# Kernel optimization log

Measured on AMD Instinct MI355X. Metric: run time of the kernel, lower is better.

The kernel has to match this reference:

```python
import jax, jax.numpy as jnp
import numpy as np

B, E, H, NY, NX = 16, 128, 4, 32, 32


def setup_inputs() -> dict:
    key = jax.random.key(0)
    ks = jax.random.split(key, 7)
    w = lambda k, shape: jax.random.normal(k, shape, jnp.float32) * 0.02
    return {
        "x": jax.random.normal(ks[0], (B, E, NY, NX), jnp.float32),
        "Wk": w(ks[1], (E, E)), "bk": jnp.zeros((E,), jnp.float32),
        "Wq": w(ks[2], (E, E)), "bq": jnp.zeros((E,), jnp.float32),
        "Wv": w(ks[3], (E, E)), "bv": jnp.zeros((E,), jnp.float32),
        "Wu": w(ks[4], (E, E)), "bu": jnp.zeros((E,), jnp.float32),
        "pos_enc": w(ks[5], (H, (2 * NY - 1) * (2 * NX - 1))),
    }


def _conv1x1(x, W, b):
    # 1x1 conv == channel-mixing linear: (B,C,y,x) -> (B,O,y,x)
    return jnp.einsum('bcyx,oc->boyx', x, W) + b[None, :, None, None]


def _rel_indices(ny, nx):
    y = jnp.arange(ny)
    x = jnp.arange(nx)
    y1, x1, y2, x2 = jnp.meshgrid(y, x, y, x, indexing='ij')
    idx = (y1 - y2 + ny - 1) * (2 * nx - 1) + (x1 - x2 + nx - 1)
    return idx.reshape(ny * nx, ny * nx)  # (N, N)


def reference(x, Wk, bk, Wq, bq, Wv, bv, Wu, bu, pos_enc):
    b, e, ny, nx = x.shape
    h = pos_enc.shape[0]
    hc = e // h
    n = ny * nx
    scale = hc ** (-0.5)

    keys = _conv1x1(x, Wk, bk).reshape(b, h, hc, n)
    queries = _conv1x1(x, Wq, bq).reshape(b, h, hc, n)
    values = _conv1x1(x, Wv, bv).reshape(b, h, hc, n)

    # att[b,h,k,q] = sum_c keys[b,h,c,k] * queries[b,h,c,q]
    att = jnp.einsum('bhck,bhcq->bhkq', keys, queries) * scale

    # gathered relative position bias: (H, N, N)
    idx = _rel_indices(ny, nx)
    rel = pos_enc[:, idx]
    att = att + rel[None]

    # softmax over the key axis (dim=-2), as in the original
    att = jax.nn.softmax(att, axis=-2)

    out = jnp.einsum('bhck,bhkq->bhcq', values, att).reshape(b, e, ny, nx)
    return _conv1x1(out, Wu, bu)
```

## Files before the change

kernel.cpp:

```cpp
#include <hip/hip_runtime.h>
#include <hip/hip_bf16.h>

#define BN 16
#define EN 128
#define HN 4
#define HCN 32
#define NN 1024
#define POSN 3969

typedef short short8 __attribute__((ext_vector_type(8)));
typedef float f32x4 __attribute__((ext_vector_type(4)));

#define MFMA16(a, b, c) __builtin_amdgcn_mfma_f32_16x16x32_bf16((a), (b), (c), 0, 0, 0)

union Frag {
  short8 s8;
  uint2 u2[2];
  unsigned int u[4];
  unsigned short us[8];
};

__device__ __forceinline__ unsigned short bfbits(float x) {
  union { __hip_bfloat16 h; unsigned short u; } c;
  c.h = __float2bfloat16(x);
  return c.u;
}

__device__ __forceinline__ unsigned int pk2(float lo, float hi) {
  union { __hip_bfloat162 h2; unsigned int u; } c;
  c.h2 = __float22bfloat162_rn(make_float2(lo, hi));
  return c.u;
}

__global__ __launch_bounds__(256) void conv_qkv_mfma(
    const float* __restrict__ x,
    const float* __restrict__ Wk, const float* __restrict__ bk, __hip_bfloat16* __restrict__ kb,
    const float* __restrict__ Wq, const float* __restrict__ bq, __hip_bfloat16* __restrict__ qb,
    const float* __restrict__ Wv, const float* __restrict__ bv, __hip_bfloat16* __restrict__ vb)
{
  const int z = blockIdx.z;
  const float* W; const float* bias; __hip_bfloat16* out;
  if (z == 0)      { W = Wk; bias = bk; out = kb; }
  else if (z == 1) { W = Wq; bias = bq; out = qb; }
  else             { W = Wv; bias = bv; out = vb; }

  const int n0 = blockIdx.x * 64;
  const int bb = blockIdx.y;
  const int t = threadIdx.x, w = t >> 6, l = t & 63;
  const int l15 = l & 15, lq = l >> 4;

  __shared__ unsigned short xs[64][132];

  {
    const float* xb = x + (size_t)bb * EN * NN + n0;
    const int n = t & 63, cg = (t >> 6) * 4;
#pragma unroll
    for (int i = 0; i < 8; ++i) {
      const int cb = cg + i * 16;
      float a0 = xb[(size_t)(cb + 0) * NN + n];
      float a1 = xb[(size_t)(cb + 1) * NN + n];
      float a2 = xb[(size_t)(cb + 2) * NN + n];
      float a3 = xb[(size_t)(cb + 3) * NN + n];
      uint2 v; v.x = pk2(a0, a1); v.y = pk2(a2, a3);
      *(uint2*)&xs[n][cb] = v;
    }
  }

  Frag wf[2][4];
#pragma unroll
  for (int r = 0; r < 2; ++r) {
    const int o = (w * 2 + r) * 16 + l15;
#pragma unroll
    for (int ks = 0; ks < 4; ++ks) {
      const float* wp = W + (size_t)o * EN + ks * 32 + lq * 4;
      float4 wa = *(const float4*)wp;
      float4 wb2 = *(const float4*)(wp + 16);
      Frag f;
      f.u[0] = pk2(wa.x, wa.y);  f.u[1] = pk2(wa.z, wa.w);
      f.u[2] = pk2(wb2.x, wb2.y); f.u[3] = pk2(wb2.z, wb2.w);
      wf[r][ks] = f;
    }
  }
  __syncthreads();

  f32x4 acc[2][4];
#pragma unroll
  for (int r = 0; r < 2; ++r)
#pragma unroll
    for (int nt = 0; nt < 4; ++nt) acc[r][nt] = 0.f;

#pragma unroll
  for (int ks = 0; ks < 4; ++ks) {
#pragma unroll
    for (int nt = 0; nt < 4; ++nt) {
      Frag xf;
      xf.u2[0] = *(const uint2*)&xs[nt * 16 + l15][ks * 32 + lq * 4];
      xf.u2[1] = *(const uint2*)&xs[nt * 16 + l15][ks * 32 + lq * 4 + 16];
      if (z < 2) {
        acc[0][nt] = MFMA16(wf[0][ks].s8, xf.s8, acc[0][nt]);
        acc[1][nt] = MFMA16(wf[1][ks].s8, xf.s8, acc[1][nt]);
      } else {
        acc[0][nt] = MFMA16(xf.s8, wf[0][ks].s8, acc[0][nt]);
        acc[1][nt] = MFMA16(xf.s8, wf[1][ks].s8, acc[1][nt]);
      }
    }
  }

  if (z < 2) {
#pragma unroll
    for (int r = 0; r < 2; ++r) {
      const int ob = (w * 2 + r) * 16 + lq * 4;
      const int hh = ob >> 5;
      const int pofs = hh * 32 + ((ob >> 2) & 3) * 8 + ((ob & 16) ? 4 : 0);
      float4 b4 = *(const float4*)(bias + ob);
#pragma unroll
      for (int nt = 0; nt < 4; ++nt) {
        const int n = n0 + nt * 16 + l15;
        f32x4 a = acc[r][nt];
        uint2 o2;
        o2.x = pk2(a[0] + b4.x, a[1] + b4.y);
        o2.y = pk2(a[2] + b4.z, a[3] + b4.w);
        *(uint2*)(out + (size_t)(bb * NN + n) * 128 + pofs) = o2;
      }
    }
  } else {
#pragma unroll
    for (int r = 0; r < 2; ++r) {
      const int o = (w * 2 + r) * 16 + l15;
      const int c = o & 31, hh = o >> 5;
      const float bsc = bias[o];
#pragma unroll
      for (int nt = 0; nt < 4; ++nt) {
        const int nb = n0 + nt * 16 + lq * 4;
        const int kbk = nb >> 5, k32 = nb & 31;
        const int pofs = ((k32 >> 2) & 3) * 8 + ((k32 & 16) ? 4 : 0);
        f32x4 a = acc[r][nt];
        uint2 o2;
        o2.x = pk2(a[0] + bsc, a[1] + bsc);
        o2.y = pk2(a[2] + bsc, a[3] + bsc);
        *(uint2*)(out + ((size_t)((bb * 4 + hh) * 32 + c) * 32 + kbk) * 32 + pofs) = o2;
      }
    }
  }
}

__global__ __launch_bounds__(256) void bias_kernel(
    const float* __restrict__ pos, unsigned short* __restrict__ bias)
{
  const int gid = blockIdx.x * 256 + threadIdx.x;
  const int l = gid & 63;
  const int t2 = gid >> 6;
  const int dxi = t2 % 3;
  const int dy31 = (t2 / 3) % 63;
  const int h = t2 / 189;
  const int rowk0 = (l >> 4) * 4, colq = l & 15;
  const float log2e = 1.4426950408889634f;

  unsigned int bits[4];
#pragma unroll
  for (int j = 0; j < 4; ++j) {
    const int dx = (dxi - 1) * 16 + rowk0 + j - colq + 31;
    bits[j] = (unsigned int)bfbits(pos[h * POSN + dy31 * 63 + dx] * log2e);
  }
  uint2 o;
  o.x = bits[0] | (bits[1] << 16);
  o.y = bits[2] | (bits[3] << 16);
  *(uint2*)(bias + (size_t)gid * 4) = o;
}

__global__ __launch_bounds__(256, 4) void attn_mfma_kernel(
    const __hip_bfloat16* __restrict__ kp,
    const __hip_bfloat16* __restrict__ qp,
    const __hip_bfloat16* __restrict__ vp,
    const unsigned short* __restrict__ bias,
    float* __restrict__ Op,
    float* __restrict__ lp)
{
  const int bx = blockIdx.x;
  const int qi = bx & 7, s = bx >> 3;
  const int h = blockIdx.y, b = blockIdx.z;
  const int t = threadIdx.x, w = t >> 6, l = t & 63;
  const int l15 = l & 15, lq = l >> 4;

  __shared__ Frag Kf[2][4][64];
  __shared__ Frag Vf[2][4][64];

  const __hip_bfloat16* kStage = kp + (size_t)b * 131072 + h * 32 + lq * 8
                                 + (size_t)(w * 16 + l15) * 128;
  const __hip_bfloat16* vStage = vp + (size_t)(b * 4 + h) * 32768
                                 + (size_t)((w >> 1) * 16 + l15) * 1024
                                 + (w & 1) * 32 + lq * 8;
  const unsigned short* biasB = bias + (size_t)h * 48384 + l * 4;

  const int qt0 = qi * 8 + w * 2;
  Frag qf[2];
  qf[0] = *(const Frag*)(qp + (size_t)(b * 1024 + (qt0 + 0) * 16 + l15) * 128 + h * 32 + lq * 8);
  qf[1] = *(const Frag*)(qp + (size_t)(b * 1024 + (qt0 + 1) * 16 + l15) * 128 + h * 32 + lq * 8);
  const int qy[2] = {(qt0 + 0) >> 1, (qt0 + 1) >> 1};
  const int qx1[2] = {(qt0 + 0) & 1, (qt0 + 1) & 1};

  {
    const int chg = s * 8;
    Kf[0][w][l] = *(const Frag*)(kStage + (size_t)chg * 64 * 128);
    Vf[0][w][l] = *(const Frag*)(vStage + chg * 64);
  }
  __syncthreads();

  f32x4 O[2][2];
#pragma unroll
  for (int mt = 0; mt < 2; ++mt)
#pragma unroll
    for (int nt = 0; nt < 2; ++nt) O[mt][nt] = 0.f;
  float lacc[2] = {0.f, 0.f};

  const float SCALE2 = 0.17677669529663687f * 1.4426950408889634f;

  for (int c8 = 0; c8 < 8; ++c8) {
    const int buf = c8 & 1;
    const int chg = s * 8 + c8;

    Frag kn, vn;
    if (c8 < 7) {
      kn = *(const Frag*)(kStage + (size_t)(chg + 1) * 64 * 128);
      vn = *(const Frag*)(vStage + (chg + 1) * 64);
    }

    uint2 bw[2][4];
#pragma unroll
    for (int nt = 0; nt < 2; ++nt)
#pragma unroll
      for (int kt = 0; kt < 4; ++kt) {
        const int ktg = chg * 4 + kt;
        const int off = ((ktg >> 1) - qy[nt] + 31) * 768 + ((ktg & 1) - qx1[nt] + 1) * 256;
        bw[nt][kt] = *(const uint2*)(biasB + off);
      }

    short8 ka[4], va[4];
#pragma unroll
    for (int kt = 0; kt < 4; ++kt) ka[kt] = Kf[buf][kt][l].s8;
#pragma unroll
    for (int i = 0; i < 4; ++i) va[i] = Vf[buf][i][l].s8;

#pragma unroll
    for (int nt = 0; nt < 2; ++nt) {
      f32x4 S[4];
#pragma unroll
      for (int kt = 0; kt < 4; ++kt) {
        f32x4 z = 0.f;
        S[kt] = MFMA16(ka[kt], qf[nt].s8, z);
      }
      float p[16];
#pragma unroll
      for (int kt = 0; kt < 4; ++kt) {
        const float b0 = __uint_as_float(bw[nt][kt].x << 16);
        const float b1 = __uint_as_float(bw[nt][kt].x & 0xffff0000u);
        const float b2 = __uint_as_float(bw[nt][kt].y << 16);
        const float b3 = __uint_as_float(bw[nt][kt].y & 0xffff0000u);
        p[kt * 4 + 0] = exp2f(fmaf(S[kt][0], SCALE2, b0));
        p[kt * 4 + 1] = exp2f(fmaf(S[kt][1], SCALE2, b1));
        p[kt * 4 + 2] = exp2f(fmaf(S[kt][2], SCALE2, b2));
        p[kt * 4 + 3] = exp2f(fmaf(S[kt][3], SCALE2, b3));
      }
#pragma unroll
      for (int e = 0; e < 16; ++e) lacc[nt] += p[e];

      Frag B0, B1;
      B0.u[0] = pk2(p[0], p[1]);   B0.u[1] = pk2(p[2], p[3]);
      B0.u[2] = pk2(p[4], p[5]);   B0.u[3] = pk2(p[6], p[7]);
      B1.u[0] = pk2(p[8], p[9]);   B1.u[1] = pk2(p[10], p[11]);
      B1.u[2] = pk2(p[12], p[13]); B1.u[3] = pk2(p[14], p[15]);

      O[0][nt] = MFMA16(va[0], B0.s8, O[0][nt]);
      O[0][nt] = MFMA16(va[1], B1.s8, O[0][nt]);
      O[1][nt] = MFMA16(va[2], B0.s8, O[1][nt]);
      O[1][nt] = MFMA16(va[3], B1.s8, O[1][nt]);
    }

    if (c8 < 7) {
      Kf[buf ^ 1][w][l] = kn;
      Vf[buf ^ 1][w][l] = vn;
      __syncthreads();
    }
  }

#pragma unroll
  for (int nt = 0; nt < 2; ++nt) {
    lacc[nt] += __shfl_xor(lacc[nt], 16);
    lacc[nt] += __shfl_xor(lacc[nt], 32);
  }
  if (lq == 0) {
#pragma unroll
    for (int nt = 0; nt < 2; ++nt)
      lp[((size_t)(s * 16 + b) * 4 + h) * 1024 + (qt0 + nt) * 16 + l15] = lacc[nt];
  }

  float* ob = Op + (size_t)s * 2097152 + ((size_t)b * EN + h * HCN) * NN;
#pragma unroll
  for (int mt = 0; mt < 2; ++mt)
#pragma unroll
    for (int nt = 0; nt < 2; ++nt)
#pragma unroll
      for (int j = 0; j < 4; ++j)
        ob[(size_t)(mt * 16 + lq * 4 + j) * NN + (qt0 + nt) * 16 + l15] = O[mt][nt][j];
}

__global__ __launch_bounds__(256) void conv_final_mfma(
    const float* __restrict__ Op,
    const float* __restrict__ lp,
    const float* __restrict__ Wu, const float* __restrict__ bu,
    float* __restrict__ out)
{
  const int n0 = blockIdx.x * 32;
  const int bb = blockIdx.y;
  const int t = threadIdx.x, w = t >> 6, l = t & 63;
  const int l15 = l & 15, lq = l >> 4;

  __shared__ unsigned short ahi[32][132];
  __shared__ unsigned short alo[32][132];

  {
    const float* O0 = Op + (size_t)bb * (EN * NN) + n0;
    const float* O1 = O0 + 2097152;
    const float* l0 = lp + (size_t)bb * 4096 + n0;
    const float* l1 = l0 + 65536;
    const int n = t & 31, cg = (t >> 5) * 4;
#pragma unroll
    for (int i = 0; i < 4; ++i) {
      const int cb = cg + i * 32;
      const float rl = 1.0f / (l0[i * 1024 + n] + l1[i * 1024 + n]);
      float a[4]; unsigned short hb[4]; float lf[4];
#pragma unroll
      for (int j = 0; j < 4; ++j) {
        a[j] = (O0[(size_t)(cb + j) * NN + n] + O1[(size_t)(cb + j) * NN + n]) * rl;
        __hip_bfloat16 hh = __float2bfloat16(a[j]);
        union { __hip_bfloat16 h; unsigned short u; } c; c.h = hh;
        hb[j] = c.u;
        lf[j] = a[j] - __bfloat162float(hh);
      }
      uint2 uh; uh.x = hb[0] | ((unsigned int)hb[1] << 16);
                uh.y = hb[2] | ((unsigned int)hb[3] << 16);
      uint2 ul; ul.x = pk2(lf[0], lf[1]); ul.y = pk2(lf[2], lf[3]);
      *(uint2*)&ahi[n][cb] = uh;
      *(uint2*)&alo[n][cb] = ul;
    }
  }

  Frag whi[2][4], wlo[2][4];
#pragma unroll
  for (int r = 0; r < 2; ++r) {
    const int o = (w * 2 + r) * 16 + l15;
#pragma unroll
    for (int ks = 0; ks < 4; ++ks) {
      const float* wp = Wu + (size_t)o * EN + ks * 32 + lq * 4;
      float4 wa = *(const float4*)wp;
      float4 wb2 = *(const float4*)(wp + 16);
      float v[8] = {wa.x, wa.y, wa.z, wa.w, wb2.x, wb2.y, wb2.z, wb2.w};
      unsigned short hb[8]; float lf[8];
#pragma unroll
      for (int e = 0; e < 8; ++e) {
        __hip_bfloat16 hh = __float2bfloat16(v[e]);
        union { __hip_bfloat16 h; unsigned short u; } c; c.h = hh;
        hb[e] = c.u;
        lf[e] = v[e] - __bfloat162float(hh);
      }
      Frag fh, fl;
#pragma unroll
      for (int e = 0; e < 4; ++e)
        fh.u[e] = hb[2 * e] | ((unsigned int)hb[2 * e + 1] << 16);
      fl.u[0] = pk2(lf[0], lf[1]); fl.u[1] = pk2(lf[2], lf[3]);
      fl.u[2] = pk2(lf[4], lf[5]); fl.u[3] = pk2(lf[6], lf[7]);
      whi[r][ks] = fh; wlo[r][ks] = fl;
    }
  }
  __syncthreads();

  f32x4 acc[2][2];
#pragma unroll
  for (int r = 0; r < 2; ++r)
#pragma unroll
    for (int nt = 0; nt < 2; ++nt) acc[r][nt] = 0.f;

#pragma unroll
  for (int ks = 0; ks < 4; ++ks) {
#pragma unroll
    for (int nt = 0; nt < 2; ++nt) {
      Frag ah, al;
      ah.u2[0] = *(const uint2*)&ahi[nt * 16 + l15][ks * 32 + lq * 4];
      ah.u2[1] = *(const uint2*)&ahi[nt * 16 + l15][ks * 32 + lq * 4 + 16];
      al.u2[0] = *(const uint2*)&alo[nt * 16 + l15][ks * 32 + lq * 4];
      al.u2[1] = *(const uint2*)&alo[nt * 16 + l15][ks * 32 + lq * 4 + 16];
#pragma unroll
      for (int r = 0; r < 2; ++r) {
        acc[r][nt] = MFMA16(ah.s8, whi[r][ks].s8, acc[r][nt]);
        acc[r][nt] = MFMA16(al.s8, whi[r][ks].s8, acc[r][nt]);
        acc[r][nt] = MFMA16(ah.s8, wlo[r][ks].s8, acc[r][nt]);
      }
    }
  }

#pragma unroll
  for (int r = 0; r < 2; ++r) {
    const int o = (w * 2 + r) * 16 + l15;
    const float bo = bu[o];
#pragma unroll
    for (int nt = 0; nt < 2; ++nt) {
      const int nb = n0 + nt * 16 + lq * 4;
      f32x4 a = acc[r][nt];
      float4 res = make_float4(a[0] + bo, a[1] + bo, a[2] + bo, a[3] + bo);
      *(float4*)(out + ((size_t)bb * EN + o) * NN + nb) = res;
    }
  }
}

extern "C" void kernel_launch(void* const* d_in, const int* in_sizes, int n_in,
                              void* d_out, int out_size, void* d_ws, size_t ws_size,
                              hipStream_t stream)
{
  const float* x   = (const float*)d_in[0];
  const float* Wk  = (const float*)d_in[1];
  const float* bk  = (const float*)d_in[2];
  const float* Wq  = (const float*)d_in[3];
  const float* bq  = (const float*)d_in[4];
  const float* Wv  = (const float*)d_in[5];
  const float* bv  = (const float*)d_in[6];
  const float* Wu  = (const float*)d_in[7];
  const float* bu  = (const float*)d_in[8];
  const float* pos = (const float*)d_in[9];

  char* ws = (char*)d_ws;
  __hip_bfloat16* kb = (__hip_bfloat16*)(ws);
  __hip_bfloat16* qb = (__hip_bfloat16*)(ws + (size_t)4194304);
  __hip_bfloat16* vb = (__hip_bfloat16*)(ws + (size_t)8388608);
  unsigned short* bias = (unsigned short*)(ws + (size_t)12582912);
  float* lp = (float*)(ws + (size_t)13107200);
  float* Op = (float*)(ws + (size_t)13631488);

  bias_kernel<<<189, 256, 0, stream>>>(pos, bias);

  dim3 g1(16, BN, 3);
  conv_qkv_mfma<<<g1, 256, 0, stream>>>(x, Wk, bk, kb, Wq, bq, qb, Wv, bv, vb);

  dim3 g2(16, HN, BN);
  attn_mfma_kernel<<<g2, 256, 0, stream>>>(kb, qb, vb, bias, Op, lp);

  dim3 g3(32, BN);
  conv_final_mfma<<<g3, 256, 0, stream>>>(Op, lp, Wu, bu, (float*)d_out);
}
```

Measured before the change: 63.64 us.

## Precompute weight fragments in prep kernel and compute softmax denominator with MFMA

Measured after the change: 58.11 us. 8.7% less time.

```diff
diff --git a/kernel.cpp b/kernel.cpp
--- a/kernel.cpp
+++ b/kernel.cpp
@@ -32,17 +32,82 @@
   return c.u;
 }
 
+__global__ __launch_bounds__(256) void prep_kernel(
+    const float* __restrict__ pos,
+    const float* __restrict__ Wk, const float* __restrict__ Wq,
+    const float* __restrict__ Wv, const float* __restrict__ Wu,
+    unsigned short* __restrict__ bias, Frag* __restrict__ wtab,
+    Frag* __restrict__ whitab, Frag* __restrict__ wlotab)
+{
+  const int b0 = blockIdx.x, t = threadIdx.x;
+  if (b0 < 189) {
+    const int gid = b0 * 256 + t;
+    const int l = gid & 63;
+    const int t2 = gid >> 6;
+    const int dxi = t2 % 3;
+    const int dy31 = (t2 / 3) % 63;
+    const int h = t2 / 189;
+    const int rowk0 = (l >> 4) * 4, colq = l & 15;
+    const float log2e = 1.4426950408889634f;
+    unsigned int bits[4];
+#pragma unroll
+    for (int j = 0; j < 4; ++j) {
+      const int dx = (dxi - 1) * 16 + rowk0 + j - colq + 31;
+      bits[j] = (unsigned int)bfbits(pos[h * POSN + dy31 * 63 + dx] * log2e);
+    }
+    uint2 o;
+    o.x = bits[0] | (bits[1] << 16);
+    o.y = bits[2] | (bits[3] << 16);
+    *(uint2*)(bias + (size_t)gid * 4) = o;
+  } else if (b0 < 213) {
+    const int fid = (b0 - 189) * 256 + t;
+    const int z = fid >> 11, rem = fid & 2047;
+    const int ot = rem >> 8, ks = (rem >> 6) & 3, l = rem & 63;
+    const float* W = (z == 0) ? Wk : (z == 1) ? Wq : Wv;
+    const int o = ot * 16 + (l & 15), lq = l >> 4;
+    const float* wp = W + (size_t)o * EN + ks * 32 + lq * 4;
+    float4 wa = *(const float4*)wp;
+    float4 wb2 = *(const float4*)(wp + 16);
+    Frag f;
+    f.u[0] = pk2(wa.x, wa.y);   f.u[1] = pk2(wa.z, wa.w);
+    f.u[2] = pk2(wb2.x, wb2.y); f.u[3] = pk2(wb2.z, wb2.w);
+    wtab[fid] = f;
+  } else {
+    const int fid = (b0 - 213) * 256 + t;
+    const int ot = fid >> 8, ks = (fid >> 6) & 3, l = fid & 63;
+    const int o = ot * 16 + (l & 15), lq = l >> 4;
+    const float* wp = Wu + (size_t)o * EN + ks * 32 + lq * 4;
+    float4 wa = *(const float4*)wp;
+    float4 wb2 = *(const float4*)(wp + 16);
+    float v[8] = {wa.x, wa.y, wa.z, wa.w, wb2.x, wb2.y, wb2.z, wb2.w};
+    unsigned short hb[8]; float lf[8];
+#pragma unroll
+    for (int e = 0; e < 8; ++e) {
+      __hip_bfloat16 hh = __float2bfloat16(v[e]);
+      union { __hip_bfloat16 h; unsigned short u; } c; c.h = hh;
+      hb[e] = c.u;
+      lf[e] = v[e] - __bfloat162float(hh);
+    }
+    Frag fh, fl;
+#pragma unroll
+    for (int e = 0; e < 4; ++e)
+      fh.u[e] = hb[2 * e] | ((unsigned int)hb[2 * e + 1] << 16);
+    fl.u[0] = pk2(lf[0], lf[1]); fl.u[1] = pk2(lf[2], lf[3]);
+    fl.u[2] = pk2(lf[4], lf[5]); fl.u[3] = pk2(lf[6], lf[7]);
+    whitab[fid] = fh;
+    wlotab[fid] = fl;
+  }
+}
+
 __global__ __launch_bounds__(256) void conv_qkv_mfma(
-    const float* __restrict__ x,
-    const float* __restrict__ Wk, const float* __restrict__ bk, __hip_bfloat16* __restrict__ kb,
-    const float* __restrict__ Wq, const float* __restrict__ bq, __hip_bfloat16* __restrict__ qb,
-    const float* __restrict__ Wv, const float* __restrict__ bv, __hip_bfloat16* __restrict__ vb)
+    const float* __restrict__ x, const Frag* __restrict__ wtab,
+    const float* __restrict__ bk, __hip_bfloat16* __restrict__ kb,
+    const float* __restrict__ bq, __hip_bfloat16* __restrict__ qb,
+    const float* __restrict__ bv, __hip_bfloat16* __restrict__ vb)
 {
   const int z = blockIdx.z;
-  const float* W; const float* bias; __hip_bfloat16* out;
-  if (z == 0)      { W = Wk; bias = bk; out = kb; }
-  else if (z == 1) { W = Wq; bias = bq; out = qb; }
-  else             { W = Wv; bias = bv; out = vb; }
+  const float* bias = (z == 0) ? bk : (z == 1) ? bq : bv;
+  __hip_bfloat16* out = (z == 0) ? kb : (z == 1) ? qb : vb;
 
   const int n0 = blockIdx.x * 64;
   const int bb = blockIdx.y;
@@ -68,19 +133,10 @@
 
   Frag wf[2][4];
 #pragma unroll
-  for (int r = 0; r < 2; ++r) {
-    const int o = (w * 2 + r) * 16 + l15;
-#pragma unroll
-    for (int ks = 0; ks < 4; ++ks) {
-      const float* wp = W + (size_t)o * EN + ks * 32 + lq * 4;
-      float4 wa = *(const float4*)wp;
-      float4 wb2 = *(const float4*)(wp + 16);
-      Frag f;
-      f.u[0] = pk2(wa.x, wa.y);  f.u[1] = pk2(wa.z, wa.w);
-      f.u[2] = pk2(wb2.x, wb2.y); f.u[3] = pk2(wb2.z, wb2.w);
-      wf[r][ks] = f;
-    }
-  }
+  for (int r = 0; r < 2; ++r)
+#pragma unroll
+    for (int ks = 0; ks < 4; ++ks)
+      wf[r][ks] = wtab[(((size_t)z * 8 + (w * 2 + r)) * 4 + ks) * 64 + l];
   __syncthreads();
 
   f32x4 acc[2][4];
@@ -142,30 +198,6 @@
       }
     }
   }
-}
-
-__global__ __launch_bounds__(256) void bias_kernel(
-    const float* __restrict__ pos, unsigned short* __restrict__ bias)
-{
-  const int gid = blockIdx.x * 256 + threadIdx.x;
-  const int l = gid & 63;
-  const int t2 = gid >> 6;
-  const int dxi = t2 % 3;
-  const int dy31 = (t2 / 3) % 63;
-  const int h = t2 / 189;
-  const int rowk0 = (l >> 4) * 4, colq = l & 15;
-  const float log2e = 1.4426950408889634f;
-
-  unsigned int bits[4];
-#pragma unroll
-  for (int j = 0; j < 4; ++j) {
-    const int dx = (dxi - 1) * 16 + rowk0 + j - colq + 31;
-    bits[j] = (unsigned int)bfbits(pos[h * POSN + dy31 * 63 + dx] * log2e);
-  }
-  uint2 o;
-  o.x = bits[0] | (bits[1] << 16);
-  o.y = bits[2] | (bits[3] << 16);
-  *(uint2*)(bias + (size_t)gid * 4) = o;
 }
 
 __global__ __launch_bounds__(256, 4) void attn_mfma_kernel(
@@ -182,15 +214,15 @@
   const int t = threadIdx.x, w = t >> 6, l = t & 63;
   const int l15 = l & 15, lq = l >> 4;
 
-  __shared__ Frag Kf[2][4][64];
-  __shared__ Frag Vf[2][4][64];
-
-  const __hip_bfloat16* kStage = kp + (size_t)b * 131072 + h * 32 + lq * 8
-                                 + (size_t)(w * 16 + l15) * 128;
-  const __hip_bfloat16* vStage = vp + (size_t)(b * 4 + h) * 32768
-                                 + (size_t)((w >> 1) * 16 + l15) * 1024
-                                 + (w & 1) * 32 + lq * 8;
+  __shared__ Frag Kf[2][8][64];
+  __shared__ Frag Vf[2][8][64];
+
+  const __hip_bfloat16* kBase = kp + (size_t)b * 131072 + h * 32 + (size_t)l15 * 128 + lq * 8;
+  const __hip_bfloat16* vBase = vp + (size_t)((b * 4 + h) * 32 + l15) * 1024 + lq * 8;
   const unsigned short* biasB = bias + (size_t)h * 48384 + l * 4;
+
+#define KADDR(CHG, KT) ((const Frag*)(kBase + (size_t)((CHG) * 128 + (KT) * 16) * 128))
+#define VADDR(CHG, SL) ((const Frag*)(vBase + (size_t)((SL) >> 2) * 16384 + ((CHG) * 4 + ((SL) & 3)) * 32))
 
   const int qt0 = qi * 8 + w * 2;
   Frag qf[2];
@@ -200,9 +232,11 @@
   const int qx1[2] = {(qt0 + 0) & 1, (qt0 + 1) & 1};
 
   {
-    const int chg = s * 8;
-    Kf[0][w][l] = *(const Frag*)(kStage + (size_t)chg * 64 * 128);
-    Vf[0][w][l] = *(const Frag*)(vStage + chg * 64);
+    const int chg = s * 4;
+    Kf[0][w][l]     = *KADDR(chg, w);
+    Kf[0][w + 4][l] = *KADDR(chg, w + 4);
+    Vf[0][w][l]     = *VADDR(chg, w);
+    Vf[0][w + 4][l] = *VADDR(chg, w + 4);
   }
   __syncthreads();
 
@@ -211,87 +245,98 @@
   for (int mt = 0; mt < 2; ++mt)
 #pragma unroll
     for (int nt = 0; nt < 2; ++nt) O[mt][nt] = 0.f;
-  float lacc[2] = {0.f, 0.f};
+  f32x4 Lacc[2]; Lacc[0] = 0.f; Lacc[1] = 0.f;
+
+  Frag ones;
+  ones.u[0] = 0x3F803F80u; ones.u[1] = 0x3F803F80u;
+  ones.u[2] = 0x3F803F80u; ones.u[3] = 0x3F803F80u;
 
   const float SCALE2 = 0.17677669529663687f * 1.4426950408889634f;
 
-  for (int c8 = 0; c8 < 8; ++c8) {
-    const int buf = c8 & 1;
-    const int chg = s * 8 + c8;
-
-    Frag kn, vn;
-    if (c8 < 7) {
-      kn = *(const Frag*)(kStage + (size_t)(chg + 1) * 64 * 128);
-      vn = *(const Frag*)(vStage + (chg + 1) * 64);
-    }
-
-    uint2 bw[2][4];
+  for (int c4 = 0; c4 < 4; ++c4) {
+    const int buf = c4 & 1;
+    const int chg = s * 4 + c4;
+
+    Frag kn[2], vn[2];
+    if (c4 < 3) {
+      kn[0] = *KADDR(chg + 1, w);
+      kn[1] = *KADDR(chg + 1, w + 4);
+      vn[0] = *VADDR(chg + 1, w);
+      vn[1] = *VADDR(chg + 1, w + 4);
+    }
+
+#pragma unroll
+    for (int hh2 = 0; hh2 < 2; ++hh2) {
+      short8 ka[4], va[4];
+#pragma unroll
+      for (int kt = 0; kt < 4; ++kt) ka[kt] = Kf[buf][hh2 * 4 + kt][l].s8;
+#pragma unroll
+      for (int mt = 0; mt < 2; ++mt)
+#pragma unroll
+        for (int kh = 0; kh < 2; ++kh)
+          va[mt * 2 + kh] = Vf[buf][mt * 4 + hh2 * 2 + kh][l].s8;
+
+#pragma unroll
+      for (int nt = 0; nt < 2; ++nt) {
+        uint2 bw[4];
+#pragma unroll
+        for (int kt = 0; kt < 4; ++kt) {
+          const int ktg = chg * 8 + hh2 * 4 + kt;
+          const int off = ((ktg >> 1) - qy[nt] + 31) * 768 + ((ktg & 1) - qx1[nt] + 1) * 256;
+          bw[kt] = *(const uint2*)(biasB + off);
+        }
+
+        __builtin_amdgcn_s_setprio(1);
+        f32x4 S[4];
+#pragma unroll
+        for (int kt = 0; kt < 4; ++kt) {
+          f32x4 z = 0.f;
+          S[kt] = MFMA16(ka[kt], qf[nt].s8, z);
+        }
+        __builtin_amdgcn_s_setprio(0);
+
+        Frag B0, B1;
+#pragma unroll
+        for (int kt = 0; kt < 4; ++kt) {
+          const float b0 = __uint_as_float(bw[kt].x << 16);
+          const float b1 = __uint_as_float(bw[kt].x & 0xffff0000u);
+          const float b2 = __uint_as_float(bw[kt].y << 16);
+          const float b3 = __uint_as_float(bw[kt].y & 0xffff0000u);
+          float p0 = exp2f(fmaf(S[kt][0], SCALE2, b0));
+          float p1 = exp2f(fmaf(S[kt][1], SCALE2, b1));
+          float p2 = exp2f(fmaf(S[kt][2], SCALE2, b2));
+          float p3 = exp2f(fmaf(S[kt][3], SCALE2, b3));
+          unsigned int lo = pk2(p0, p1), hi = pk2(p2, p3);
+          if (kt < 2) { B0.u[kt * 2] = lo; B0.u[kt * 2 + 1] = hi; }
+          else        { B1.u[(kt - 2) * 2] = lo; B1.u[(kt - 2) * 2 + 1] = hi; }
+        }
+
+        __builtin_amdgcn_s_setprio(1);
+        O[0][nt] = MFMA16(va[0], B0.s8, O[0][nt]);
+        O[0][nt] = MFMA16(va[1], B1.s8, O[0][nt]);
+        O[1][nt] = MFMA16(va[2], B0.s8, O[1][nt]);
+        O[1][nt] = MFMA16(va[3], B1.s8, O[1][nt]);
+        Lacc[nt] = MFMA16(ones.s8, B0.s8, Lacc[nt]);
+        Lacc[nt] = MFMA16(ones.s8, B1.s8, Lacc[nt]);
+        __builtin_amdgcn_s_setprio(0);
+      }
+    }
+
+    if (c4 < 3) {
+      Kf[buf ^ 1][w][l]     = kn[0];
+      Kf[buf ^ 1][w + 4][l] = kn[1];
+      Vf[buf ^ 1][w][l]     = vn[0];
+      Vf[buf ^ 1][w + 4][l] = vn[1];
+      __syncthreads();
+    }
+  }
+#undef KADDR
+#undef VADDR
+
+  if (lq == 0) {
 #pragma unroll
     for (int nt = 0; nt < 2; ++nt)
-#pragma unroll
-      for (int kt = 0; kt < 4; ++kt) {
-        const int ktg = chg * 4 + kt;
-        const int off = ((ktg >> 1) - qy[nt] + 31) * 768 + ((ktg & 1) - qx1[nt] + 1) * 256;
-        bw[nt][kt] = *(const uint2*)(biasB + off);
-      }
-
-    short8 ka[4], va[4];
-#pragma unroll
-    for (int kt = 0; kt < 4; ++kt) ka[kt] = Kf[buf][kt][l].s8;
-#pragma unroll
-    for (int i = 0; i < 4; ++i) va[i] = Vf[buf][i][l].s8;
-
-#pragma unroll
-    for (int nt = 0; nt < 2; ++nt) {
-      f32x4 S[4];
-#pragma unroll
-      for (int kt = 0; kt < 4; ++kt) {
-        f32x4 z = 0.f;
-        S[kt] = MFMA16(ka[kt], qf[nt].s8, z);
-      }
-      float p[16];
-#pragma unroll
-      for (int kt = 0; kt < 4; ++kt) {
-        const float b0 = __uint_as_float(bw[nt][kt].x << 16);
-        const float b1 = __uint_as_float(bw[nt][kt].x & 0xffff0000u);
-        const float b2 = __uint_as_float(bw[nt][kt].y << 16);
-        const float b3 = __uint_as_float(bw[nt][kt].y & 0xffff0000u);
-        p[kt * 4 + 0] = exp2f(fmaf(S[kt][0], SCALE2, b0));
-        p[kt * 4 + 1] = exp2f(fmaf(S[kt][1], SCALE2, b1));
-        p[kt * 4 + 2] = exp2f(fmaf(S[kt][2], SCALE2, b2));
-        p[kt * 4 + 3] = exp2f(fmaf(S[kt][3], SCALE2, b3));
-      }
-#pragma unroll
-      for (int e = 0; e < 16; ++e) lacc[nt] += p[e];
-
-      Frag B0, B1;
-      B0.u[0] = pk2(p[0], p[1]);   B0.u[1] = pk2(p[2], p[3]);
-      B0.u[2] = pk2(p[4], p[5]);   B0.u[3] = pk2(p[6], p[7]);
-      B1.u[0] = pk2(p[8], p[9]);   B1.u[1] = pk2(p[10], p[11]);
-      B1.u[2] = pk2(p[12], p[13]); B1.u[3] = pk2(p[14], p[15]);
-
-      O[0][nt] = MFMA16(va[0], B0.s8, O[0][nt]);
-      O[0][nt] = MFMA16(va[1], B1.s8, O[0][nt]);
-      O[1][nt] = MFMA16(va[2], B0.s8, O[1][nt]);
-      O[1][nt] = MFMA16(va[3], B1.s8, O[1][nt]);
-    }
-
-    if (c8 < 7) {
-      Kf[buf ^ 1][w][l] = kn;
-      Vf[buf ^ 1][w][l] = vn;
-      __syncthreads();
-    }
-  }
-
-#pragma unroll
-  for (int nt = 0; nt < 2; ++nt) {
-    lacc[nt] += __shfl_xor(lacc[nt], 16);
-    lacc[nt] += __shfl_xor(lacc[nt], 32);
-  }
-  if (lq == 0) {
-#pragma unroll
-    for (int nt = 0; nt < 2; ++nt)
-      lp[((size_t)(s * 16 + b) * 4 + h) * 1024 + (qt0 + nt) * 16 + l15] = lacc[nt];
+      lp[((size_t)(s * 16 + b) * 4 + h) * 1024 + (qt0 + nt) * 16 + l15] = Lacc[nt][0];
   }
 
   float* ob = Op + (size_t)s * 2097152 + ((size_t)b * EN + h * HCN) * NN;
@@ -307,8 +352,8 @@
 __global__ __launch_bounds__(256) void conv_final_mfma(
     const float* __restrict__ Op,
     const float* __restrict__ lp,
-    const float* __restrict__ Wu, const float* __restrict__ bu,
-    float* __restrict__ out)
+    const Frag* __restrict__ whitab, const Frag* __restrict__ wlotab,
+    const float* __restrict__ bu, float* __restrict__ out)
 {
   const int n0 = blockIdx.x * 32;
   const int bb = blockIdx.y;
@@ -347,31 +392,13 @@
 
   Frag whi[2][4], wlo[2][4];
 #pragma unroll
-  for (int r = 0; r < 2; ++r) {
-    const int o = (w * 2 + r) * 16 + l15;
+  for (int r = 0; r < 2; ++r)
 #pragma unroll
     for (int ks = 0; ks < 4; ++ks) {
-      const float* wp = Wu + (size_t)o * EN + ks * 32 + lq * 4;
-      float4 wa = *(const float4*)wp;
-      float4 wb2 = *(const float4*)(wp + 16);
-      float v[8] = {wa.x, wa.y, wa.z, wa.w, wb2.x, wb2.y, wb2.z, wb2.w};
-      unsigned short hb[8]; float lf[8];
-#pragma unroll
-      for (int e = 0; e < 8; ++e) {
-        __hip_bfloat16 hh = __float2bfloat16(v[e]);
-        union { __hip_bfloat16 h; unsigned short u; } c; c.h = hh;
-        hb[e] = c.u;
-        lf[e] = v[e] - __bfloat162float(hh);
-      }
-      Frag fh, fl;
-#pragma unroll
-      for (int e = 0; e < 4; ++e)
-        fh.u[e] = hb[2 * e] | ((unsigned int)hb[2 * e + 1] << 16);
-      fl.u[0] = pk2(lf[0], lf[1]); fl.u[1] = pk2(lf[2], lf[3]);
-      fl.u[2] = pk2(lf[4], lf[5]); fl.u[3] = pk2(lf[6], lf[7]);
-      whi[r][ks] = fh; wlo[r][ks] = fl;
-    }
-  }
+      const int idx = (((w * 2 + r) * 4) + ks) * 64 + l;
+      whi[r][ks] = whitab[idx];
+      wlo[r][ks] = wlotab[idx];
+    }
   __syncthreads();
 
   f32x4 acc[2][2];
@@ -432,17 +459,20 @@
   __hip_bfloat16* qb = (__hip_bfloat16*)(ws + (size_t)4194304);
   __hip_bfloat16* vb = (__hip_bfloat16*)(ws + (size_t)8388608);
   unsigned short* bias = (unsigned short*)(ws + (size_t)12582912);
-  float* lp = (float*)(ws + (size_t)13107200);
-  float* Op = (float*)(ws + (size_t)13631488);
-
-  bias_kernel<<<189, 256, 0, stream>>>(pos, bias);
+  Frag* wtab   = (Frag*)(ws + (size_t)12969984);
+  Frag* whitab = (Frag*)(ws + (size_t)13068288);
+  Frag* wlotab = (Frag*)(ws + (size_t)13101056);
+  float* lp = (float*)(ws + (size_t)13133824);
+  float* Op = (float*)(ws + (size_t)13658112);
+
+  prep_kernel<<<221, 256, 0, stream>>>(pos, Wk, Wq, Wv, Wu, bias, wtab, whitab, wlotab);
 
   dim3 g1(16, BN, 3);
-  conv_qkv_mfma<<<g1, 256, 0, stream>>>(x, Wk, bk, kb, Wq, bq, qb, Wv, bv, vb);
+  conv_qkv_mfma<<<g1, 256, 0, stream>>>(x, wtab, bk, kb, bq, qb, bv, vb);
 
   dim3 g2(16, HN, BN);
   attn_mfma_kernel<<<g2, 256, 0, stream>>>(kb, qb, vb, bias, Op, lp);
 
   dim3 g3(32, BN);
-  conv_final_mfma<<<g3, 256, 0, stream>>>(Op, lp, Wu, bu, (float*)d_out);
-}
+  conv_final_mfma<<<g3, 256, 0, stream>>>(Op, lp, whitab, wlotab, bu, (float*)d_out);
+}
```
